# Kernel optimization log

Hardware: AMD Instinct MI355X
Metric: run time of the kernel (lower is better)

## Reference

```python
import jax, jax.numpy as jnp
import numpy as np

S, B, I = 256, 64, 1024   # seqlen, batch, input_size
H = 1024                   # hidden_size
P_LEN, P = 256, 1024       # post seqlen, post_size
NEG = -1000000000.0


def setup_inputs() -> dict:
    key = jax.random.key(0)
    ks = jax.random.split(key, 11)
    sc = 0.03
    return {
        "incoming": jax.random.normal(ks[0], (S, B, I), jnp.float32),
        "post": jax.random.normal(ks[1], (P_LEN, B, P), jnp.float32),
        "h_init": jax.random.normal(ks[2], (1, 1, H), jnp.float32) * sc,
        "W_ih": jax.random.normal(ks[3], (3 * H, I), jnp.float32) * sc,
        "W_hh": jax.random.normal(ks[4], (3 * H, H), jnp.float32) * sc,
        "b_ih": jax.random.normal(ks[5], (3 * H,), jnp.float32) * sc,
        "b_hh": jax.random.normal(ks[6], (3 * H,), jnp.float32) * sc,
        "Wq": jax.random.normal(ks[7], (P, H), jnp.float32) * sc,
        "bq": jax.random.normal(ks[8], (P,), jnp.float32) * sc,
        "length": jnp.maximum(jax.random.randint(ks[9], (B,), 0, S), 1),
        "post_length": jnp.maximum(jax.random.randint(ks[10], (B,), 0, P_LEN), 1),
    }


def reference(incoming, post, h_init, W_ih, W_hh, b_ih, b_hh, Wq, bq, length, post_length):
    seqlen, batch = incoming.shape[0], incoming.shape[1]
    post_seqlen = post.shape[0]
    dt = incoming.dtype
    # per-step keep mask: (length > i)  -> [S, B, 1]
    keep = (jnp.arange(seqlen)[:, None] < length[None, :]).astype(dt)[..., None]
    # post mask: arange(post_seqlen) < post_length -> [P_LEN, B]
    pmask = jnp.arange(post_seqlen)[:, None] < post_length[None, :]

    h0 = jnp.broadcast_to(h_init[0], (batch, h_init.shape[-1])).astype(dt)

    def step(h, inp):
        x, k = inp  # x: [B, I], k: [B, 1]
        gi = x @ W_ih.T + b_ih          # [B, 3H]
        gh = h @ W_hh.T + b_hh          # [B, 3H]
        i_r, i_z, i_n = jnp.split(gi, 3, axis=-1)
        h_r, h_z, h_n = jnp.split(gh, 3, axis=-1)
        r = jax.nn.sigmoid(i_r + h_r)
        z = jax.nn.sigmoid(i_z + h_z)
        n = jnp.tanh(i_n + r * h_n)
        h_new = (n + z * (h - n)) * k   # GRUCell then zero out past-length steps
        query = h_new @ Wq.T + bq       # [B, P]
        scores = jnp.einsum('bp,lbp->lb', query, post)  # [P_LEN, B]
        scores = jnp.where(pmask, scores, NEG)
        attn = jax.nn.softmax(scores, axis=0)           # softmax over post seq
        context = jnp.einsum('lb,lbp->bp', attn, post)  # [B, P]
        return h_new, (jnp.concatenate([h_new, context], axis=-1), attn)
    h_last, (hs, attn_weights) = jax.lax.scan(step, h0, (incoming, keep))
    return h_last, hs, attn_weights
```

## Files before the change

### kernel.cpp

```cpp
#include <hip/hip_runtime.h>
#include <cstdio>
#include <cstdint>
#include <math.h>

typedef float vf4 __attribute__((ext_vector_type(4)));

constexpr int SEQ = 256, BATCH = 64, HID = 1024, TH3 = 3072, PLEN = 256;
constexpr float NEGV = -1000000000.0f;

constexpr int GI_CHUNK = 8;
constexpr int Q_CHUNK  = 32;

constexpr size_t OFF_H  = 1024;
constexpr size_t OFF_GI = OFF_H + 2 * 1024 * 64;
constexpr size_t GI_FLOATS = (size_t)GI_CHUNK * TH3 * BATCH;
constexpr size_t WS_NEED = (OFF_GI + 2 * GI_FLOATS) * sizeof(float);

__device__ __forceinline__ void gbar(unsigned* bar) {
  __syncthreads();
  if (threadIdx.x == 0) {
    const unsigned e = __hip_atomic_load(&bar[544], __ATOMIC_RELAXED, __HIP_MEMORY_SCOPE_AGENT);
    const int g = blockIdx.x & 31;
    const unsigned o = __hip_atomic_fetch_add(&bar[g * 16], 1u, __ATOMIC_RELAXED, __HIP_MEMORY_SCOPE_AGENT);
    bool last = false;
    if (o == 7u) {
      const unsigned r = __hip_atomic_fetch_add(&bar[512], 1u, __ATOMIC_RELAXED, __HIP_MEMORY_SCOPE_AGENT);
      if (r == 31u) {
#pragma unroll
        for (int i = 0; i < 32; ++i)
          __hip_atomic_store(&bar[i * 16], 0u, __ATOMIC_RELAXED, __HIP_MEMORY_SCOPE_AGENT);
        __hip_atomic_store(&bar[512], 0u, __ATOMIC_RELAXED, __HIP_MEMORY_SCOPE_AGENT);
        __hip_atomic_fetch_add(&bar[544], 1u, __ATOMIC_RELEASE, __HIP_MEMORY_SCOPE_AGENT);
        last = true;
      }
    }
    if (!last) {
      while (__hip_atomic_load(&bar[544], __ATOMIC_RELAXED, __HIP_MEMORY_SCOPE_AGENT) == e)
        __builtin_amdgcn_s_sleep(8);
    }
    (void)__hip_atomic_load(&bar[544], __ATOMIC_ACQUIRE, __HIP_MEMORY_SCOPE_AGENT);
  }
  __syncthreads();
}

__global__ __launch_bounds__(256, 2)
void k_fused(const float* __restrict__ incoming, const float* __restrict__ post,
             const float* __restrict__ h_init, const float* __restrict__ W_ih,
             const float* __restrict__ W_hh, const float* __restrict__ b_ih,
             const float* __restrict__ b_hh, const float* __restrict__ Wq,
             const float* __restrict__ bq, const int* __restrict__ length,
             const int* __restrict__ post_length, float* __restrict__ out,
             float* __restrict__ ws, int rec_s0, int last_chunk,
             int gi_c, int q_qc, int at_qc)
{
  __shared__ float lds[16384];
  int bid = blockIdx.x;
  const int tid = threadIdx.x;

  if (rec_s0 >= 0) {
    if (bid < 256) {
      float* Wl = lds;
      float* hs = lds + 12288;
      unsigned* bar = (unsigned*)ws;
      const int wg = bid;
      const int wave = tid >> 6, lane = tid & 63;
      float* out_hs = out + (size_t)BATCH * HID;
      const float* gip = ws + OFF_GI + (size_t)((rec_s0 >> 3) & 1) * GI_FLOATS;

      for (int t = tid; t < 3072; t += 256) {
        const int r = t >> 8, kq = t & 255;
        const int grow = (r >> 2) * 1024 + wg * 4 + (r & 3);
        *(vf4*)&Wl[r * 1024 + kq * 4] = *(const vf4*)&W_hh[(size_t)grow * HID + kq * 4];
      }
      const int lb = length[lane];
      const float bh0 = b_hh[0 * 1024 + wg * 4 + wave];
      const float bh1 = b_hh[1 * 1024 + wg * 4 + wave];
      const float bh2 = b_hh[2 * 1024 + wg * 4 + wave];
      const int j = wg * 4 + wave;
      if (rec_s0 == 0) {
        __hip_atomic_store(&(ws + OFF_H)[j * 64 + lane], h_init[j],
                           __ATOMIC_RELAXED, __HIP_MEMORY_SCOPE_AGENT);
        gbar(bar);
      } else {
        __syncthreads();
      }

      for (int s = rec_s0; s < rec_s0 + GI_CHUNK; ++s) {
        const float* hT = ws + OFF_H + (size_t)(s & 1) * 65536;
        float* hTn = ws + OFF_H + (size_t)((s + 1) & 1) * 65536;
        const size_t gib = (size_t)(s - rec_s0) * (TH3 * 64);
        const float gi_r = gip[gib + (size_t)(0 * 1024 + j) * 64 + lane];
        const float gi_z = gip[gib + (size_t)(1 * 1024 + j) * 64 + lane];
        const float gi_n = gip[gib + (size_t)(2 * 1024 + j) * 64 + lane];
        const float hold = hT[(size_t)j * 64 + lane];
        float acc[12];
#pragma unroll
        for (int r = 0; r < 12; ++r) acc[r] = 0.f;

        vf4 rbuf[4];
        {
          const vf4* src = (const vf4*)hT;
#pragma unroll
          for (int j4 = 0; j4 < 4; ++j4) rbuf[j4] = src[tid + 256 * j4];
        }
        for (int kt = 0; kt < 16; ++kt) {
          vf4* dst = (vf4*)hs;
#pragma unroll
          for (int j4 = 0; j4 < 4; ++j4) dst[tid + 256 * j4] = rbuf[j4];
          __syncthreads();
          if (kt < 15) {
            const vf4* src = (const vf4*)(hT + (kt + 1) * 4096);
#pragma unroll
            for (int j4 = 0; j4 < 4; ++j4) rbuf[j4] = src[tid + 256 * j4];
          }
#pragma unroll
          for (int kq = 0; kq < 4; ++kq) {
            const int kk = wave * 16 + kq * 4;
            vf4 wv[12];
#pragma unroll
            for (int r = 0; r < 12; ++r)
              wv[r] = *(const vf4*)&Wl[r * 1024 + kt * 64 + kk];
            float hv[4];
#pragma unroll
            for (int i = 0; i < 4; ++i) hv[i] = hs[(kk + i) * 64 + lane];
#pragma unroll
            for (int i = 0; i < 4; ++i) {
              const float hvi = hv[i];
#pragma unroll
              for (int r = 0; r < 12; ++r) acc[r] = fmaf(hvi, wv[r][i], acc[r]);
            }
          }
          __syncthreads();
        }
#pragma unroll
        for (int r = 0; r < 12; ++r) hs[wave * 768 + r * 64 + lane] = acc[r];
        __syncthreads();
        float gsum[3];
#pragma unroll
        for (int g = 0; g < 3; ++g) {
          const int r = g * 4 + wave;
          gsum[g] = hs[r * 64 + lane] + hs[768 + r * 64 + lane] +
                    hs[1536 + r * 64 + lane] + hs[2304 + r * 64 + lane];
        }
        const float rg = 1.f / (1.f + expf(-(gi_r + gsum[0] + bh0)));
        const float zg = 1.f / (1.f + expf(-(gi_z + gsum[1] + bh1)));
        const float ng = tanhf(gi_n + rg * (gsum[2] + bh2));
        const float keep = (s < lb) ? 1.f : 0.f;
        const float hn = (ng + zg * (hold - ng)) * keep;
        __hip_atomic_store(&hTn[(size_t)j * 64 + lane], hn,
                           __ATOMIC_RELAXED, __HIP_MEMORY_SCOPE_AGENT);
        hs[3328 + lane * 4 + wave] = hn;
        __syncthreads();
        if (tid < 64)
          *(vf4*)&out_hs[(size_t)s * (BATCH * 2048) + (size_t)tid * 2048 + wg * 4] =
              *(vf4*)&hs[3328 + tid * 4];
        if (last_chunk && s == rec_s0 + GI_CHUNK - 1) {
          out[(size_t)lane * HID + j] = hn;
        } else if (s < rec_s0 + GI_CHUNK - 1) {
          gbar(bar);
        }
      }
      return;
    }
    bid -= 256;
  }

  if (gi_c >= 0) {
    if (bid < 192) {
      float* Wt = lds;
      float* Xs = lds + 4096;
      const int rt = bid % 24, sl = bid / 24;
      const int s = gi_c * GI_CHUNK + sl;
      const int mq = tid & 31, bq_ = tid >> 5;
      const int m0 = rt * 128;
      const float* Xg = incoming + (size_t)s * (BATCH * HID);
      float* gid = ws + OFF_GI + (size_t)(gi_c & 1) * GI_FLOATS;
      float acc[4][8];
#pragma unroll
      for (int jj = 0; jj < 4; ++jj)
#pragma unroll
        for (int i = 0; i < 8; ++i) acc[jj][i] = 0.f;

      for (int kt = 0; kt < 32; ++kt) {
        const int k0 = kt * 32;
        {
          const int row = tid >> 1, half = tid & 1;
          const float* srcp = W_ih + (size_t)(m0 + row) * HID + k0 + half * 16;
#pragma unroll
          for (int f = 0; f < 4; ++f) {
            vf4 v = *(const vf4*)(srcp + f * 4);
            const int kb = half * 16 + f * 4;
            Wt[(kb + 0) * 128 + row] = v[0];
            Wt[(kb + 1) * 128 + row] = v[1];
            Wt[(kb + 2) * 128 + row] = v[2];
            Wt[(kb + 3) * 128 + row] = v[3];
          }
        }
        {
          const int bb = tid >> 2, kq = tid & 3;
          const float* srcp = Xg + (size_t)bb * HID + k0;
#pragma unroll
          for (int hh = 0; hh < 2; ++hh) {
            const int slot = kq + hh * 4;
            vf4 v = *(const vf4*)(srcp + slot * 4);
            Xs[(slot * 4 + 0) * 64 + bb] = v[0];
            Xs[(slot * 4 + 1) * 64 + bb] = v[1];
            Xs[(slot * 4 + 2) * 64 + bb] = v[2];
            Xs[(slot * 4 + 3) * 64 + bb] = v[3];
          }
        }
        __syncthreads();
#pragma unroll 4
        for (int kk = 0; kk < 32; ++kk) {
          vf4 x0 = *(const vf4*)&Xs[kk * 64 + bq_ * 8];
          vf4 x1 = *(const vf4*)&Xs[kk * 64 + bq_ * 8 + 4];
          float wv[4];
#pragma unroll
          for (int jj = 0; jj < 4; ++jj) wv[jj] = Wt[kk * 128 + mq + 32 * jj];
#pragma unroll
          for (int jj = 0; jj < 4; ++jj) {
            acc[jj][0] = fmaf(wv[jj], x0[0], acc[jj][0]);
            acc[jj][1] = fmaf(wv[jj], x0[1], acc[jj][1]);
            acc[jj][2] = fmaf(wv[jj], x0[2], acc[jj][2]);
            acc[jj][3] = fmaf(wv[jj], x0[3], acc[jj][3]);
            acc[jj][4] = fmaf(wv[jj], x1[0], acc[jj][4]);
            acc[jj][5] = fmaf(wv[jj], x1[1], acc[jj][5]);
            acc[jj][6] = fmaf(wv[jj], x1[2], acc[jj][6]);
            acc[jj][7] = fmaf(wv[jj], x1[3], acc[jj][7]);
          }
        }
        __syncthreads();
      }
#pragma unroll
      for (int jj = 0; jj < 4; ++jj) {
        const int m = m0 + mq + 32 * jj;
        const float bm = b_ih[m];
        float* dst = gid + (size_t)sl * (TH3 * 64) + (size_t)m * 64 + bq_ * 8;
        vf4 o0 = {acc[jj][0] + bm, acc[jj][1] + bm, acc[jj][2] + bm, acc[jj][3] + bm};
        vf4 o1 = {acc[jj][4] + bm, acc[jj][5] + bm, acc[jj][6] + bm, acc[jj][7] + bm};
        *(vf4*)dst = o0;
        *(vf4*)(dst + 4) = o1;
      }
      return;
    }
    bid -= 192;
  }

  if (q_qc >= 0) {
    if (bid < 512) {
      float* Wt = lds;
      float* Ht = lds + 4096;
      const int pt = bid & 7, b = bid >> 3;
      const int s0q = q_qc * Q_CHUNK;
      const float* Hbase = out + (size_t)BATCH * HID;
      float* outq = out + (size_t)BATCH * HID;
      const int pq = tid & 31, sq = tid >> 5;
      const int p0 = pt * 128;
      float acc[4][4];
#pragma unroll
      for (int i = 0; i < 4; ++i)
#pragma unroll
        for (int jj = 0; jj < 4; ++jj) acc[i][jj] = 0.f;

      for (int kt = 0; kt < 32; ++kt) {
        const int k0 = kt * 32;
        {
          const int row = tid >> 1, half = tid & 1;
          const float* srcp = Wq + (size_t)(p0 + row) * HID + k0 + half * 16;
#pragma unroll
          for (int f = 0; f < 4; ++f) {
            vf4 v = *(const vf4*)(srcp + f * 4);
            const int kb = half * 16 + f * 4;
            Wt[(kb + 0) * 128 + row] = v[0];
            Wt[(kb + 1) * 128 + row] = v[1];
            Wt[(kb + 2) * 128 + row] = v[2];
            Wt[(kb + 3) * 128 + row] = v[3];
          }
        }
        {
          const int sl = tid >> 3, slot = tid & 7;
          vf4 v = *(const vf4*)&Hbase[(size_t)(s0q + sl) * (BATCH * 2048) + (size_t)b * 2048 + k0 + slot * 4];
          Ht[(slot * 4 + 0) * 32 + sl] = v[0];
          Ht[(slot * 4 + 1) * 32 + sl] = v[1];
          Ht[(slot * 4 + 2) * 32 + sl] = v[2];
          Ht[(slot * 4 + 3) * 32 + sl] = v[3];
        }
        __syncthreads();
#pragma unroll 4
        for (int kk = 0; kk < 32; ++kk) {
          vf4 hv = *(const vf4*)&Ht[kk * 32 + sq * 4];
          vf4 wv = *(const vf4*)&Wt[kk * 128 + pq * 4];
#pragma unroll
          for (int si = 0; si < 4; ++si)
#pragma unroll
            for (int pi = 0; pi < 4; ++pi) acc[si][pi] = fmaf(hv[si], wv[pi], acc[si][pi]);
        }
        __syncthreads();
      }
      vf4 bqv = *(const vf4*)&bq[p0 + pq * 4];
#pragma unroll
      for (int si = 0; si < 4; ++si) {
        vf4 o = {acc[si][0] + bqv[0], acc[si][1] + bqv[1], acc[si][2] + bqv[2], acc[si][3] + bqv[3]};
        *(vf4*)&outq[(size_t)(s0q + sq * 4 + si) * (BATCH * 2048) + (size_t)b * 2048 + 1024 + p0 + pq * 4] = o;
      }
      return;
    }
    bid -= 512;
  }

  if (at_qc >= 0 && bid < 256) {
    float* q8   = lds;
    float* Pt   = lds + 8192;
    float* sc   = lds + 12416;
    float* stat = lds + 14464;
    const int b = bid & 63, st = bid >> 6;
    const int wave = tid >> 6, lane = tid & 63;
    const int plen = post_length[b];
    const int sbase = at_qc * Q_CHUNK + st * 8;
    float* out_hs = out + (size_t)BATCH * HID;
    float* out_attn = out_hs + (size_t)SEQ * BATCH * 2048;

    {
#pragma unroll
      for (int i = 0; i < 8; ++i) {
        const float* srcr = out_hs + (size_t)(sbase + i) * (BATCH * 2048) + (size_t)b * 2048 + 1024;
        *(vf4*)&q8[i * 1024 + tid * 4] = *(const vf4*)&srcr[tid * 4];
      }
    }
    __syncthreads();

    const int l32 = tid & 31, sq = tid >> 5;
    for (int lt = 0; lt < 8; ++lt) {
      const int l0 = lt * 32;
      if (l0 < plen) {
        float a = 0.f;
        for (int ptile = 0; ptile < 8; ++ptile) {
#pragma unroll
          for (int i = 0; i < 4; ++i) {
            const int f4i = tid + 256 * i;
            const int row = f4i >> 5, c4 = f4i & 31;
            *(vf4*)&Pt[row * 132 + c4 * 4] =
                *(const vf4*)&post[(size_t)(l0 + row) * (BATCH * HID) + (size_t)b * HID + ptile * 128 + c4 * 4];
          }
          __syncthreads();
#pragma unroll 8
          for (int p4 = 0; p4 < 32; ++p4) {
            vf4 qv = *(const vf4*)&q8[sq * 1024 + ptile * 128 + p4 * 4];
            vf4 pv = *(const vf4*)&Pt[l32 * 132 + p4 * 4];
            a = fmaf(qv[0], pv[0], a);
            a = fmaf(qv[1], pv[1], a);
            a = fmaf(qv[2], pv[2], a);
            a = fmaf(qv[3], pv[3], a);
          }
          __syncthreads();
        }
        sc[sq * 256 + l0 + l32] = (l0 + l32 < plen) ? a : NEGV;
      } else {
        sc[sq * 256 + l0 + l32] = NEGV;
      }
    }
    __syncthreads();

    for (int si = wave; si < 8; si += 4) {
      float v0 = sc[si * 256 + lane], v1 = sc[si * 256 + 64 + lane];
      float v2 = sc[si * 256 + 128 + lane], v3 = sc[si * 256 + 192 + lane];
      float m = fmaxf(fmaxf(v0, v1), fmaxf(v2, v3));
#pragma unroll
      for (int off = 32; off > 0; off >>= 1) m = fmaxf(m, __shfl_xor(m, off));
      float e0 = expf(v0 - m), e1 = expf(v1 - m), e2 = expf(v2 - m), e3 = expf(v3 - m);
      float ssum = e0 + e1 + e2 + e3;
#pragma unroll
      for (int off = 32; off > 0; off >>= 1) ssum += __shfl_xor(ssum, off);
      sc[si * 256 + lane] = e0;
      sc[si * 256 + 64 + lane] = e1;
      sc[si * 256 + 128 + lane] = e2;
      sc[si * 256 + 192 + lane] = e3;
      if (lane == 0) stat[si] = 1.f / ssum;
    }
    __syncthreads();

#pragma unroll
    for (int i = 0; i < 8; ++i) {
      const int idx = tid + 256 * i;
      const int si = idx >> 8, l = idx & 255;
      out_attn[(size_t)(sbase + si) * (PLEN * BATCH) + (size_t)l * BATCH + b] = sc[si * 256 + l] * stat[si];
    }

    vf4 a[8];
#pragma unroll
    for (int s8 = 0; s8 < 8; ++s8) a[s8] = (vf4){0.f, 0.f, 0.f, 0.f};
    const int lr = (plen + 3) & ~3;
    for (int l = 0; l < lr; l += 4) {
      vf4 w[8];
#pragma unroll
      for (int s8 = 0; s8 < 8; ++s8) w[s8] = *(const vf4*)&sc[s8 * 256 + l];
#pragma unroll
      for (int u = 0; u < 4; ++u) {
        vf4 pv = *(const vf4*)&post[(size_t)(l + u) * (BATCH * HID) + (size_t)b * HID + tid * 4];
#pragma unroll
        for (int s8 = 0; s8 < 8; ++s8) a[s8] = a[s8] + pv * w[s8][u];
      }
    }
#pragma unroll
    for (int s8 = 0; s8 < 8; ++s8) {
      vf4 r = a[s8] * stat[s8];
      *(vf4*)&out_hs[(size_t)(sbase + s8) * (BATCH * 2048) + (size_t)b * 2048 + 1024 + tid * 4] = r;
    }
  }
}

extern "C" void kernel_launch(void* const* d_in, const int* in_sizes, int n_in,
                              void* d_out, int out_size, void* d_ws, size_t ws_size,
                              hipStream_t stream) {
  const float* incoming    = (const float*)d_in[0];
  const float* post        = (const float*)d_in[1];
  const float* h_init      = (const float*)d_in[2];
  const float* W_ih        = (const float*)d_in[3];
  const float* W_hh        = (const float*)d_in[4];
  const float* b_ih        = (const float*)d_in[5];
  const float* b_hh        = (const float*)d_in[6];
  const float* Wq          = (const float*)d_in[7];
  const float* bq          = (const float*)d_in[8];
  const int*   length      = (const int*)d_in[9];
  const int*   post_length = (const int*)d_in[10];
  float* out = (float*)d_out;
  float* ws  = (float*)d_ws;

  if (ws_size < WS_NEED) {
    fprintf(stderr, "[gru_attn] ERROR: ws too small (%zu < %zu)\n", ws_size, WS_NEED);
    return;
  }
  hipMemsetAsync(d_ws, 0, 4096, stream);

  hipLaunchKernelGGL(k_fused, dim3(192), dim3(256), 0, stream,
                     incoming, post, h_init, W_ih, W_hh, b_ih, b_hh, Wq, bq,
                     length, post_length, out, ws,
                     -1, 0, 0, -1, -1);

  for (int c = 0; c <= 33; ++c) {
    const int rec_s0 = (c < 32) ? c * GI_CHUNK : -1;
    const int last   = (c == 31) ? 1 : 0;
    const int gi_c   = (c >= 0 && c < 31) ? c + 1 : -1;
    int q_qc = -1, at_qc = -1;
    if (c >= 4 && c <= 28 && (c & 3) == 0) q_qc = c / 4 - 1;
    if (c == 32) q_qc = 7;
    if (c >= 5 && c <= 29 && (c & 3) == 1) at_qc = (c - 5) / 4;
    if (c == 33) at_qc = 7;
    const int nb = (rec_s0 >= 0 ? 256 : 0) + (gi_c >= 0 ? 192 : 0) +
                   (q_qc >= 0 ? 512 : 0) + (at_qc >= 0 ? 256 : 0);
    if (nb == 0) continue;
    hipLaunchKernelGGL(k_fused, dim3(nb), dim3(256), 0, stream,
                       incoming, post, h_init, W_ih, W_hh, b_ih, b_hh, Wq, bq,
                       length, post_length, out, ws,
                       rec_s0, last, gi_c, q_qc, at_qc);
  }
}
```

Before: 7.128 ms.

## Stream W_hh from global in recurrence and size LDS dynamically per launch

The recurrent blocks no longer stage their W_hh slice into LDS. Each wave now reads the hidden state directly from global memory with a double-buffered register prefetch, and reads weights straight from global, relying on the cache. Shared memory becomes dynamic and is sized per launch from the roles present, launch bounds are raised to four blocks per CU, and the recurrence waves get higher scheduling priority. The aim is more co-resident blocks and no per-step LDS staging or syncs, at the cost of more global and cache traffic for weights on every step and tighter register limits.

```diff
diff --git a/kernel.cpp b/kernel.cpp
--- a/kernel.cpp
+++ b/kernel.cpp
@@ -15,6 +15,11 @@
 constexpr size_t OFF_GI = OFF_H + 2 * 1024 * 64;
 constexpr size_t GI_FLOATS = (size_t)GI_CHUNK * TH3 * BATCH;
 constexpr size_t WS_NEED = (OFF_GI + 2 * GI_FLOATS) * sizeof(float);
+
+constexpr unsigned LDS_REC = 3584u * 4;
+constexpr unsigned LDS_GI  = 6144u * 4;
+constexpr unsigned LDS_Q   = 5120u * 4;
+constexpr unsigned LDS_AT  = 14472u * 4;
 
 __device__ __forceinline__ void gbar(unsigned* bar) {
   __syncthreads();
@@ -43,7 +48,7 @@
   __syncthreads();
 }
 
-__global__ __launch_bounds__(256, 2)
+__global__ __launch_bounds__(256, 4)
 void k_fused(const float* __restrict__ incoming, const float* __restrict__ post,
              const float* __restrict__ h_init, const float* __restrict__ W_ih,
              const float* __restrict__ W_hh, const float* __restrict__ b_ih,
@@ -53,25 +58,22 @@
              float* __restrict__ ws, int rec_s0, int last_chunk,
              int gi_c, int q_qc, int at_qc)
 {
-  __shared__ float lds[16384];
+  extern __shared__ float lds[];
   int bid = blockIdx.x;
   const int tid = threadIdx.x;
 
   if (rec_s0 >= 0) {
     if (bid < 256) {
-      float* Wl = lds;
-      float* hs = lds + 12288;
+      float* red = lds;
       unsigned* bar = (unsigned*)ws;
       const int wg = bid;
-      const int wave = tid >> 6, lane = tid & 63;
+      const int wave = __builtin_amdgcn_readfirstlane(tid >> 6);
+      const int lane = tid & 63;
       float* out_hs = out + (size_t)BATCH * HID;
       const float* gip = ws + OFF_GI + (size_t)((rec_s0 >> 3) & 1) * GI_FLOATS;
 
-      for (int t = tid; t < 3072; t += 256) {
-        const int r = t >> 8, kq = t & 255;
-        const int grow = (r >> 2) * 1024 + wg * 4 + (r & 3);
-        *(vf4*)&Wl[r * 1024 + kq * 4] = *(const vf4*)&W_hh[(size_t)grow * HID + kq * 4];
-      }
+      __builtin_amdgcn_s_setprio(1);
+
       const int lb = length[lane];
       const float bh0 = b_hh[0 * 1024 + wg * 4 + wave];
       const float bh1 = b_hh[1 * 1024 + wg * 4 + wave];
@@ -81,8 +83,6 @@
         __hip_atomic_store(&(ws + OFF_H)[j * 64 + lane], h_init[j],
                            __ATOMIC_RELAXED, __HIP_MEMORY_SCOPE_AGENT);
         gbar(bar);
-      } else {
-        __syncthreads();
       }
 
       for (int s = rec_s0; s < rec_s0 + GI_CHUNK; ++s) {
@@ -97,50 +97,45 @@
 #pragma unroll
         for (int r = 0; r < 12; ++r) acc[r] = 0.f;
 
-        vf4 rbuf[4];
-        {
-          const vf4* src = (const vf4*)hT;
-#pragma unroll
-          for (int j4 = 0; j4 < 4; ++j4) rbuf[j4] = src[tid + 256 * j4];
-        }
-        for (int kt = 0; kt < 16; ++kt) {
-          vf4* dst = (vf4*)hs;
-#pragma unroll
-          for (int j4 = 0; j4 < 4; ++j4) dst[tid + 256 * j4] = rbuf[j4];
-          __syncthreads();
-          if (kt < 15) {
-            const vf4* src = (const vf4*)(hT + (kt + 1) * 4096);
-#pragma unroll
-            for (int j4 = 0; j4 < 4; ++j4) rbuf[j4] = src[tid + 256 * j4];
-          }
-#pragma unroll
-          for (int kq = 0; kq < 4; ++kq) {
-            const int kk = wave * 16 + kq * 4;
-            vf4 wv[12];
-#pragma unroll
-            for (int r = 0; r < 12; ++r)
-              wv[r] = *(const vf4*)&Wl[r * 1024 + kt * 64 + kk];
-            float hv[4];
-#pragma unroll
-            for (int i = 0; i < 4; ++i) hv[i] = hs[(kk + i) * 64 + lane];
-#pragma unroll
-            for (int i = 0; i < 4; ++i) {
-              const float hvi = hv[i];
-#pragma unroll
-              for (int r = 0; r < 12; ++r) acc[r] = fmaf(hvi, wv[r][i], acc[r]);
-            }
-          }
-          __syncthreads();
-        }
-#pragma unroll
-        for (int r = 0; r < 12; ++r) hs[wave * 768 + r * 64 + lane] = acc[r];
+#define LOADH(dst, ktv)                                                         \
+        do {                                                                    \
+          const int kb_ = (ktv) * 64 + wave * 16;                               \
+          _Pragma("unroll")                                                     \
+          for (int i_ = 0; i_ < 16; ++i_)                                       \
+            dst[i_] = hT[(size_t)(kb_ + i_) * 64 + lane];                       \
+        } while (0)
+#define COMP(src, ktv)                                                          \
+        do {                                                                    \
+          const int kb_ = (ktv) * 64 + wave * 16;                               \
+          _Pragma("unroll")                                                     \
+          for (int r_ = 0; r_ < 12; ++r_) {                                     \
+            const float* Wr_ =                                                  \
+                W_hh + (size_t)((r_ >> 2) * 1024 + wg * 4 + (r_ & 3)) * 1024 + kb_; \
+            _Pragma("unroll")                                                   \
+            for (int i_ = 0; i_ < 16; ++i_)                                     \
+              acc[r_] = fmaf(src[i_], Wr_[i_], acc[r_]);                        \
+          }                                                                     \
+        } while (0)
+        float hva[16], hvb[16];
+        LOADH(hva, 0);
+        for (int kt = 0; kt < 16; kt += 2) {
+          LOADH(hvb, kt + 1);
+          COMP(hva, kt);
+          if (kt < 14) LOADH(hva, kt + 2);
+          COMP(hvb, kt + 1);
+        }
+#undef LOADH
+#undef COMP
+
+#pragma unroll
+        for (int r = 0; r < 12; ++r) red[wave * 768 + r * 64 + lane] = acc[r];
         __syncthreads();
         float gsum[3];
 #pragma unroll
         for (int g = 0; g < 3; ++g) {
           const int r = g * 4 + wave;
-          gsum[g] = hs[r * 64 + lane] + hs[768 + r * 64 + lane] +
-                    hs[1536 + r * 64 + lane] + hs[2304 + r * 64 + lane];
+          gsum[g] = red[r * 64 + lane] + red[768 + r * 64 + lane] +
+                    red[1536 + r * 64 + lane] + red[2304 + r * 64 + lane];
         }
         const float rg = 1.f / (1.f + expf(-(gi_r + gsum[0] + bh0)));
         const float zg = 1.f / (1.f + expf(-(gi_z + gsum[1] + bh1)));
@@ -149,17 +144,18 @@
         const float hn = (ng + zg * (hold - ng)) * keep;
         __hip_atomic_store(&hTn[(size_t)j * 64 + lane], hn,
                            __ATOMIC_RELAXED, __HIP_MEMORY_SCOPE_AGENT);
-        hs[3328 + lane * 4 + wave] = hn;
+        red[3328 + lane * 4 + wave] = hn;
         __syncthreads();
         if (tid < 64)
           *(vf4*)&out_hs[(size_t)s * (BATCH * 2048) + (size_t)tid * 2048 + wg * 4] =
-              *(vf4*)&hs[3328 + tid * 4];
+              *(vf4*)&red[3328 + tid * 4];
         if (last_chunk && s == rec_s0 + GI_CHUNK - 1) {
           out[(size_t)lane * HID + j] = hn;
         } else if (s < rec_s0 + GI_CHUNK - 1) {
           gbar(bar);
         }
       }
+      __builtin_amdgcn_s_setprio(0);
       return;
     }
     bid -= 256;
@@ -408,6 +404,8 @@
     }
   }
 }
+
+static inline unsigned umax(unsigned a, unsigned b) { return a > b ? a : b; }
 
 extern "C" void kernel_launch(void* const* d_in, const int* in_sizes, int n_in,
                               void* d_out, int out_size, void* d_ws, size_t ws_size,
@@ -432,7 +430,7 @@
   }
   hipMemsetAsync(d_ws, 0, 4096, stream);
 
-  hipLaunchKernelGGL(k_fused, dim3(192), dim3(256), 0, stream,
+  hipLaunchKernelGGL(k_fused, dim3(192), dim3(256), LDS_GI, stream,
                      incoming, post, h_init, W_ih, W_hh, b_ih, b_hh, Wq, bq,
                      length, post_length, out, ws,
                      -1, 0, 0, -1, -1);
@@ -449,7 +447,12 @@
     const int nb = (rec_s0 >= 0 ? 256 : 0) + (gi_c >= 0 ? 192 : 0) +
                    (q_qc >= 0 ? 512 : 0) + (at_qc >= 0 ? 256 : 0);
     if (nb == 0) continue;
-    hipLaunchKernelGGL(k_fused, dim3(nb), dim3(256), 0, stream,
+    unsigned ldsb = 0;
+    if (rec_s0 >= 0) ldsb = umax(ldsb, LDS_REC);
+    if (gi_c >= 0)   ldsb = umax(ldsb, LDS_GI);
+    if (q_qc >= 0)   ldsb = umax(ldsb, LDS_Q);
+    if (at_qc >= 0)  ldsb = umax(ldsb, LDS_AT);
+    hipLaunchKernelGGL(k_fused, dim3(nb), dim3(256), ldsb, stream,
                        incoming, post, h_init, W_ih, W_hh, b_ih, b_hh, Wq, bq,
                        length, post_length, out, ws,
                        rec_s0, last, gi_c, q_qc, at_qc);
```

Result: slower. 10.17 ms (+42.6%).
